# Optimization experiments

Hardware: AMD Instinct MI355X
Metric: run time of the kernel (lower is better)

Reference implementation:

```python
import jax, jax.numpy as jnp
import numpy as np

B, N, L = 256, 128, 2048
NF, AC, HID = 75, 3, 256
DIM, NHEAD, FPD, NWORD = 128, 8, 679, 8600


def setup_inputs() -> dict:
    key = jax.random.key(0)
    ks = iter(jax.random.split(key, 48))
    rn = lambda *s: jax.random.normal(next(ks), s, dtype=jnp.float32) * 0.05
    d = {}
    d['V'] = jax.random.normal(next(ks), (B, N, NF), dtype=jnp.float32)
    d['A'] = jax.random.uniform(next(ks), (B, AC, N, N), dtype=jnp.float32)
    d['fp'] = jax.random.uniform(next(ks), (B, FPD), dtype=jnp.float32)
    d['mol_size'] = jax.random.randint(next(ks), (B,), 1, N + 1, dtype=jnp.int32)
    d['protein_seq'] = jax.random.randint(next(ks), (B, L), 0, NWORD)
    d['label'] = jax.random.randint(next(ks), (B,), 0, 2)
    # GConv blocks (multi-channel GCN): 75->256, 256->256, 256->256
    d['gc_W1'], d['gc_b1'] = rn(AC, NF, HID), rn(HID)
    d['gc_W2'], d['gc_b2'] = rn(AC, HID, HID), rn(HID)
    d['gc_W3'], d['gc_b3'] = rn(AC, HID, HID), rn(HID)
    # fp linear chain: 679->128, 128->128
    d['fp_W1'], d['fp_b1'] = rn(FPD, DIM), rn(DIM)
    d['fp_W2'], d['fp_b2'] = rn(DIM, DIM), rn(DIM)
    # global attention pooling (per-head node scores) + readout
    d['att_W'] = rn(HID, NHEAD)
    d['ro_W'], d['ro_b'] = rn(HID * NHEAD, DIM), rn(DIM)
    d['emb'] = rn(NWORD, DIM)
    # cross-attention projections
    d['mfp_W'], d['mfp_b'] = rn(DIM, DIM), rn(DIM)
    d['pfp_W'], d['pfp_b'] = rn(DIM, DIM), rn(DIM)
    d['mv_W'], d['mv_b'] = rn(DIM, DIM), rn(DIM)
    d['pv_W'], d['pv_b'] = rn(DIM, DIM), rn(DIM)
    # stacked MLPs (3 layers each, width 2*dim)
    d['mlp1_W'], d['mlp1_b'] = rn(3, 2 * DIM, 2 * DIM), rn(3, 2 * DIM)
    d['mlp2_W'], d['mlp2_b'] = rn(3, 2 * DIM, 2 * DIM), rn(3, 2 * DIM)
    d['out1_W'], d['out1_b'] = rn(2 * DIM, 2), rn(2)
    d['out2_W'], d['out2_b'] = rn(2 * DIM, 2), rn(2)
    return d


def _gconv(V, A, W, b):
    # A: [b,c,n,m], V: [b,m,f], W: [c,f,o]
    AV = jnp.einsum('bcnm,bmf->bcnf', A, V)
    return jax.nn.relu(jnp.einsum('bcnf,cfo->bno', AV, W) + b)


def _cross_attn(hvec, prot_emb, mW, mb, pW, pb):
    # hvec: [b,d]; prot_emb: [b,l,d]
    h = jax.nn.relu(hvec @ mW + mb)                       # [b,d]
    hs = jax.nn.relu(jnp.einsum('bld,de->ble', prot_emb, pW) + pb)  # [b,l,d]
    w = jnp.tanh(jnp.einsum('bd,bld->bl', h, hs))         # [b,l]
    ys = w[..., None] * hs                                 # [b,l,d]
    return jnp.max(ys, axis=1)                             # [b,d]


def reference(V, A, fp, mol_size, protein_seq, label,
              gc_W1, gc_b1, gc_W2, gc_b2, gc_W3, gc_b3,
              fp_W1, fp_b1, fp_W2, fp_b2, att_W, ro_W, ro_b, emb,
              mfp_W, mfp_b, pfp_W, pfp_b, mv_W, mv_b, pv_W, pv_b,
              mlp1_W, mlp1_b, mlp2_W, mlp2_b, out1_W, out1_b, out2_W, out2_b):
    # fp linear chain (dropout = identity at inference)
    fp = jax.nn.relu(fp @ fp_W1 + fp_b1)
    fp = jax.nn.relu(fp @ fp_W2 + fp_b2)
    # graph conv blocks
    Vh = _gconv(V, A, gc_W1, gc_b1)
    Vh = _gconv(Vh, A, gc_W2, gc_b2)
    Vh = _gconv(Vh, A, gc_W3, gc_b3)
    # masked multi-head global attention pooling over nodes
    scores = jnp.einsum('bnf,fh->bnh', Vh, att_W)          # [b,n,heads]
    mask = jnp.arange(N)[None, :] < mol_size[:, None]       # [b,n]
    scores = jnp.where(mask[..., None], scores, -1e9)
    att = jax.nn.softmax(scores, axis=1)
    pooled = jnp.einsum('bnh,bnf->bhf', att, Vh).reshape(Vh.shape[0], -1)  # [b, heads*nf]
    Vr = jax.nn.relu(pooled @ ro_W + ro_b)                  # [b,dim]
    # protein embedding + ragged cross-attention branches
    prot_emb = emb[protein_seq]                             # [b,l,dim]
    itact1 = _cross_attn(fp, prot_emb, mfp_W, mfp_b, pfp_W, pfp_b)
    itact2 = _cross_attn(Vr, prot_emb, mv_W, mv_b, pv_W, pv_b)
    cat1 = jnp.concatenate([fp, itact1], axis=1)
    cat2 = jnp.concatenate([Vr, itact2], axis=1)
    for i in range(mlp1_W.shape[0]):
        cat1 = jax.nn.relu(cat1 @ mlp1_W[i] + mlp1_b[i])
        cat2 = jax.nn.relu(cat2 @ mlp2_W[i] + mlp2_b[i])
    pred_itact = (cat1 @ out1_W + out1_b) + (cat2 @ out2_W + out2_b)
    pred_labels = jnp.argmax(pred_itact, axis=1)
    pred_scores = jax.nn.softmax(pred_itact, axis=1)[:, 1]
    return (pred_itact, label, pred_labels, pred_scores)
```

## Files before the change

kernel.cpp:

```cpp
#include <hip/hip_runtime.h>
#include <math.h>

static constexpr int BB   = 256;
static constexpr int NN   = 128;
static constexpr int LL   = 2048;
static constexpr int NF   = 75;
static constexpr int AC   = 3;
static constexpr int HID  = 256;
static constexpr int DIM  = 128;
static constexpr int NHEAD= 8;
static constexpr int FPD  = 679;
static constexpr int FPDP = 704;
static constexpr int NWORD= 8600;
static constexpr int NWP  = 8704;
static constexpr int KB   = 768;

typedef __attribute__((ext_vector_type(8))) _Float16 f16x8;
typedef __attribute__((ext_vector_type(4))) float f32x4;
typedef unsigned int u32;
typedef unsigned short u16;

__device__ __forceinline__ u16 f2h(float x) {
    _Float16 h = (_Float16)x;
    return *(u16*)&h;
}
__device__ __forceinline__ u16 f2h_sat(float x) {
    x = fminf(fmaxf(x, -65000.f), 65000.f);
    _Float16 h = (_Float16)x;
    return *(u16*)&h;
}
__device__ __forceinline__ float h2f(u16 x) {
    return (float)(*(_Float16*)&x);
}

static constexpr float SC   = 0.0625f;
static constexpr float USC  = 16.0f;

__global__ __launch_bounds__(256)
void prepA_kernel(const float* __restrict__ A, u16* __restrict__ Ah)
{
    size_t base = (size_t)blockIdx.x * (NN * NN);
    int t = threadIdx.x;
    #pragma unroll
    for (int i = 0; i < 16; ++i) {
        int id = t + i * 256;
        float4 v = *(const float4*)(A + base + (size_t)id * 4);
        u32 p0 = (u32)f2h(v.x) | ((u32)f2h(v.y) << 16);
        u32 p1 = (u32)f2h(v.z) | ((u32)f2h(v.w) << 16);
        *(uint2*)(Ah + base + (size_t)id * 4) = make_uint2(p0, p1);
    }
}

__global__ __launch_bounds__(256)
void prepFp_kernel(const float* __restrict__ fp, u16* __restrict__ fph)
{
    int b = blockIdx.x, t = threadIdx.x;
    for (int i = t; i < FPDP; i += 256) {
        float v = (i < FPD) ? fp[(size_t)b * FPD + i] : 0.f;
        fph[(size_t)b * FPDP + i] = f2h(v);
    }
}

__global__ __launch_bounds__(256)
void prepFpW_kernel(const float* __restrict__ fpW1, const float* __restrict__ fpW2,
                    u16* __restrict__ W1t, u16* __restrict__ W2t)
{
    int o = blockIdx.x, z = blockIdx.y, t = threadIdx.x;
    if (z == 0) {
        for (int k = t; k < FPDP; k += 256) {
            float v = (k < FPD) ? fpW1[(size_t)k * DIM + o] : 0.f;
            W1t[(size_t)o * FPDP + k] = f2h(v);
        }
    } else {
        if (t < 128) W2t[(size_t)o * 128 + t] = f2h(fpW2[(size_t)t * DIM + o]);
    }
}

__global__ __launch_bounds__(128)
void prepCrossW_kernel(const float* __restrict__ pfpW, const float* __restrict__ pvW,
                       const float* __restrict__ mfpW, const float* __restrict__ mvW,
                       u16* __restrict__ pWt12, u16* __restrict__ mWt12)
{
    int o = blockIdx.x, z = blockIdx.y, t = threadIdx.x;
    const float* W = (z == 0) ? pfpW : (z == 1) ? pvW : (z == 2) ? mfpW : mvW;
    u16* Wt = (z < 2) ? (pWt12 + (size_t)z * 128 * 128)
                      : (mWt12 + (size_t)(z - 2) * 128 * 128);
    Wt[(size_t)o * 128 + t] = f2h(W[(size_t)t * 128 + o]);
}

__global__ __launch_bounds__(256)
void prepMlpW_kernel(const float* __restrict__ m1W, const float* __restrict__ m2W,
                     u16* __restrict__ Wmlp)
{
    int o = blockIdx.x, Lr = blockIdx.y, br = blockIdx.z, t = threadIdx.x;
    const float* W = (br ? m2W : m1W) + (size_t)Lr * 256 * 256;
    Wmlp[(((size_t)(br * 3 + Lr)) * 256 + o) * 256 + t] = f2h(W[(size_t)t * 256 + o]);
}

__global__ __launch_bounds__(256)
void fp1_mfma(const u16* __restrict__ fph, const u16* __restrict__ W1t,
              const float* __restrict__ b1, u16* __restrict__ FP1h)
{
    __shared__ u16 As[128 * 40];
    __shared__ u16 Bs[128 * 40];
    int mt = blockIdx.x;
    const u16* Ap = fph + (size_t)(mt * 128) * FPDP;

    int t = threadIdx.x;
    int l = t & 63, wid = t >> 6;
    int rb = (wid >> 1) * 64, cb = (wid & 1) * 64;
    int ln = l & 15, q = l >> 4;

    f32x4 acc[4][4] = {};

    for (int kt = 0; kt < FPDP / 32; ++kt) {
        #pragma unroll
        for (int i = 0; i < 2; ++i) {
            int id = t + i * 256;
            int row = id >> 2, qh = id & 3;
            *(uint4*)&As[row * 40 + qh * 8] =
                *(const uint4*)(Ap + (size_t)row * FPDP + kt * 32 + qh * 8);
            *(uint4*)&Bs[row * 40 + qh * 8] =
                *(const uint4*)(W1t + (size_t)row * FPDP + kt * 32 + qh * 8);
        }
        __syncthreads();
        f16x8 af[4], bfr[4];
        #pragma unroll
        for (int fr = 0; fr < 4; ++fr)
            af[fr] = *(const f16x8*)&As[(rb + fr * 16 + ln) * 40 + q * 8];
        #pragma unroll
        for (int fc = 0; fc < 4; ++fc)
            bfr[fc] = *(const f16x8*)&Bs[(cb + fc * 16 + ln) * 40 + q * 8];
        #pragma unroll
        for (int fr = 0; fr < 4; ++fr)
            #pragma unroll
            for (int fc = 0; fc < 4; ++fc)
                acc[fr][fc] = __builtin_amdgcn_mfma_f32_16x16x32_f16(
                    af[fr], bfr[fc], acc[fr][fc], 0, 0, 0);
        __syncthreads();
    }
    #pragma unroll
    for (int fr = 0; fr < 4; ++fr)
        #pragma unroll
        for (int fc = 0; fc < 4; ++fc) {
            int d = cb + fc * 16 + ln;
            float bv = b1[d];
            #pragma unroll
            for (int r = 0; r < 4; ++r) {
                int m = rb + fr * 16 + q * 4 + r;
                FP1h[(size_t)(mt * 128 + m) * 128 + d] = f2h(fmaxf(acc[fr][fc][r] + bv, 0.f));
            }
        }
}

__global__ __launch_bounds__(256)
void fp2_mfma(const u16* __restrict__ FP1h, const u16* __restrict__ W2t,
              const float* __restrict__ b2, float* __restrict__ FP2,
              u16* __restrict__ FP2h)
{
    __shared__ u16 As[128 * 40];
    __shared__ u16 Bs[128 * 40];
    int mt = blockIdx.x;
    const u16* Ap = FP1h + (size_t)(mt * 128) * 128;

    int t = threadIdx.x;
    int l = t & 63, wid = t >> 6;
    int rb = (wid >> 1) * 64, cb = (wid & 1) * 64;
    int ln = l & 15, q = l >> 4;

    f32x4 acc[4][4] = {};

    for (int kt = 0; kt < 4; ++kt) {
        #pragma unroll
        for (int i = 0; i < 2; ++i) {
            int id = t + i * 256;
            int row = id >> 2, qh = id & 3;
            *(uint4*)&As[row * 40 + qh * 8] =
                *(const uint4*)(Ap + (size_t)row * 128 + kt * 32 + qh * 8);
            *(uint4*)&Bs[row * 40 + qh * 8] =
                *(const uint4*)(W2t + (size_t)row * 128 + kt * 32 + qh * 8);
        }
        __syncthreads();
        f16x8 af[4], bfr[4];
        #pragma unroll
        for (int fr = 0; fr < 4; ++fr)
            af[fr] = *(const f16x8*)&As[(rb + fr * 16 + ln) * 40 + q * 8];
        #pragma unroll
        for (int fc = 0; fc < 4; ++fc)
            bfr[fc] = *(const f16x8*)&Bs[(cb + fc * 16 + ln) * 40 + q * 8];
        #pragma unroll
        for (int fr = 0; fr < 4; ++fr)
            #pragma unroll
            for (int fc = 0; fc < 4; ++fc)
                acc[fr][fc] = __builtin_amdgcn_mfma_f32_16x16x32_f16(
                    af[fr], bfr[fc], acc[fr][fc], 0, 0, 0);
        __syncthreads();
    }
    #pragma unroll
    for (int fr = 0; fr < 4; ++fr)
        #pragma unroll
        for (int fc = 0; fc < 4; ++fc) {
            int d = cb + fc * 16 + ln;
            float bv = b2[d];
            #pragma unroll
            for (int r = 0; r < 4; ++r) {
                int m = rb + fr * 16 + q * 4 + r;
                float val = fmaxf(acc[fr][fc][r] + bv, 0.f);
                FP2 [(size_t)(mt * 128 + m) * 128 + d] = val;
                FP2h[(size_t)(mt * 128 + m) * 128 + d] = f2h(val);
            }
        }
}

__global__ __launch_bounds__(256)
void hs12_mfma(const float* __restrict__ emb, const u16* __restrict__ pWt12,
               const float* __restrict__ ba, const float* __restrict__ bb_,
               u16* __restrict__ HS12)
{
    __shared__ u16 As[128 * 40];
    __shared__ u16 Bs[128 * 40];
    int ft = blockIdx.x, br = blockIdx.y;
    const u16* Bp = pWt12 + (size_t)br * 128 * 128;
    const float* bias = br ? bb_ : ba;
    int r0 = ft * 128;

    int t = threadIdx.x;
    int l = t & 63, wid = t >> 6;
    int rb = (wid >> 1) * 64, cb = (wid & 1) * 64;
    int ln = l & 15, q = l >> 4;

    f32x4 acc[4][4] = {};

    for (int kt = 0; kt < 4; ++kt) {
        #pragma unroll
        for (int i = 0; i < 4; ++i) {
            int id = t + i * 256;
            int row = id >> 3, qf = id & 7;
            int r = r0 + row;
            float4 v = make_float4(0.f, 0.f, 0.f, 0.f);
            if (r < NWORD) v = *(const float4*)(emb + (size_t)r * 128 + kt * 32 + qf * 4);
            u32 p0 = (u32)f2h(v.x) | ((u32)f2h(v.y) << 16);
            u32 p1 = (u32)f2h(v.z) | ((u32)f2h(v.w) << 16);
            u32* dst = (u32*)&As[row * 40 + qf * 4];
            dst[0] = p0; dst[1] = p1;
        }
        #pragma unroll
        for (int i = 0; i < 2; ++i) {
            int id = t + i * 256;
            int row = id >> 2, qh = id & 3;
            *(uint4*)&Bs[row * 40 + qh * 8] =
                *(const uint4*)(Bp + (size_t)row * 128 + kt * 32 + qh * 8);
        }
        __syncthreads();
        f16x8 af[4], bfr[4];
        #pragma unroll
        for (int fr = 0; fr < 4; ++fr)
            af[fr] = *(const f16x8*)&As[(rb + fr * 16 + ln) * 40 + q * 8];
        #pragma unroll
        for (int fc = 0; fc < 4; ++fc)
            bfr[fc] = *(const f16x8*)&Bs[(cb + fc * 16 + ln) * 40 + q * 8];
        #pragma unroll
        for (int fr = 0; fr < 4; ++fr)
            #pragma unroll
            for (int fc = 0; fc < 4; ++fc)
                acc[fr][fc] = __builtin_amdgcn_mfma_f32_16x16x32_f16(
                    af[fr], bfr[fc], acc[fr][fc], 0, 0, 0);
        __syncthreads();
    }
    #pragma unroll
    for (int fr = 0; fr < 4; ++fr)
        #pragma unroll
        for (int fc = 0; fc < 4; ++fc) {
            int d = cb + fc * 16 + ln;
            float bv = bias[d];
            #pragma unroll
            for (int r = 0; r < 4; ++r) {
                int m = rb + fr * 16 + q * 4 + r;
                int rr = r0 + m;
                if (rr < NWORD)
                    HS12[(size_t)rr * 256 + br * 128 + d] = f2h(fmaxf(acc[fr][fc][r] + bv, 0.f));
            }
        }
}

__global__ __launch_bounds__(256)
void prepVt_kernel(const float* __restrict__ V, u16* __restrict__ Vt)
{
    int b = blockIdx.x, t = threadIdx.x;
    __shared__ float sV[NN * NF];
    for (int i = t; i < NN * NF; i += 256) sV[i] = V[(size_t)b * (NN * NF) + i];
    __syncthreads();
    for (int i = t; i < 80 * 128; i += 256) {
        int f = i >> 7, n = i & 127;
        float v = (f < NF) ? sV[n * NF + f] : 0.f;
        Vt[(size_t)b * (80 * 128) + i] = f2h(v);
    }
}

__global__ __launch_bounds__(256)
void prepW_kernel(const float* __restrict__ W1, const float* __restrict__ W2,
                  const float* __restrict__ W3, u16* __restrict__ Wt1,
                  u16* __restrict__ Wt2, u16* __restrict__ Wt3)
{
    int o = blockIdx.x, z = blockIdx.y, t = threadIdx.x;
    if (z == 0) {
        int k = t;
        int c = k / 80, f = k - c * 80;
        float v = (c < 3 && f < NF) ? W1[((size_t)c * NF + f) * HID + o] : 0.f;
        Wt1[(size_t)o * 256 + k] = f2h(v);
    } else {
        const float* W = (z == 1) ? W2 : W3;
        u16* Wt = (z == 1) ? Wt2 : Wt3;
        for (int k = t; k < KB; k += 256) {
            int c = k >> 8, f = k & 255;
            Wt[(size_t)o * KB + k] = f2h(W[((size_t)c * HID + f) * HID + o]);
        }
    }
}

__global__ __launch_bounds__(256)
void transp_kernel(const u16* __restrict__ H, u16* __restrict__ Ht)
{
    __shared__ u16 s[32][34];
    int o0 = blockIdx.x * 32, n0 = blockIdx.y * 32, b = blockIdx.z;
    int tx = threadIdx.x & 31, ty = threadIdx.x >> 5;
    const u16* Hp = H + (size_t)b * (NN * HID);
    #pragma unroll
    for (int j = 0; j < 4; ++j)
        s[ty + 8 * j][tx] = Hp[(size_t)(n0 + ty + 8 * j) * HID + o0 + tx];
    __syncthreads();
    u16* Hto = Ht + (size_t)b * (HID * NN);
    #pragma unroll
    for (int j = 0; j < 4; ++j)
        Hto[(size_t)(o0 + ty + 8 * j) * NN + n0 + tx] = s[tx][ty + 8 * j];
}

__global__ __launch_bounds__(256)
void gA_mfma(const u16* __restrict__ Agr, const u16* __restrict__ Htr,
             u16* __restrict__ AV, int b0, int htStride, int fpMul, int Fvalid)
{
    __shared__ u16 As[128 * 40];
    __shared__ u16 Bs[128 * 40];
    int ft = blockIdx.x, c = blockIdx.y, bl = blockIdx.z;
    int b = b0 + bl;
    const u16* Ap = Agr + ((size_t)b * AC + c) * (NN * NN);
    const u16* Bp = Htr + (size_t)b * htStride + ft * (128 * 128);
    u16* Cp = AV + (size_t)bl * (NN * KB) + c * fpMul + ft * 128;

    int t = threadIdx.x;
    int l = t & 63, wid = t >> 6;
    int rb = (wid >> 1) * 64, cb = (wid & 1) * 64;
    int ln = l & 15, q = l >> 4;

    f32x4 acc[4][4] = {};

    for (int kt = 0; kt < 4; ++kt) {
        #pragma unroll
        for (int i = 0; i < 2; ++i) {
            int id = t + i * 256;
            int row = id >> 2, qh = id & 3;
            *(uint4*)&As[row * 40 + qh * 8] =
                *(const uint4*)(Ap + (size_t)row * NN + kt * 32 + qh * 8);
        }
        #pragma unroll
        for (int i = 0; i < 2; ++i) {
            int id = t + i * 256;
            int row = id >> 2, qh = id & 3;
            uint4 v = make_uint4(0, 0, 0, 0);
            if (row < Fvalid) v = *(const uint4*)(Bp + (size_t)row * 128 + kt * 32 + qh * 8);
            *(uint4*)&Bs[row * 40 + qh * 8] = v;
        }
        __syncthreads();
        f16x8 af[4], bfr[4];
        #pragma unroll
        for (int fr = 0; fr < 4; ++fr)
            af[fr] = *(const f16x8*)&As[(rb + fr * 16 + ln) * 40 + q * 8];
        #pragma unroll
        for (int fc = 0; fc < 4; ++fc)
            bfr[fc] = *(const f16x8*)&Bs[(cb + fc * 16 + ln) * 40 + q * 8];
        #pragma unroll
        for (int fr = 0; fr < 4; ++fr)
            #pragma unroll
            for (int fc = 0; fc < 4; ++fc)
                acc[fr][fc] = __builtin_amdgcn_mfma_f32_16x16x32_f16(
                    af[fr], bfr[fc], acc[fr][fc], 0, 0, 0);
        __syncthreads();
    }
    #pragma unroll
    for (int fr = 0; fr < 4; ++fr) {
        #pragma unroll
        for (int fc = 0; fc < 4; ++fc) {
            int fcol = cb + fc * 16 + ln;
            if (fcol < Fvalid) {
                #pragma unroll
                for (int r = 0; r < 4; ++r) {
                    int n = rb + fr * 16 + q * 4 + r;
                    Cp[(size_t)n * KB + fcol] = f2h_sat(acc[fr][fc][r] * SC);
                }
            }
        }
    }
}

__global__ __launch_bounds__(256)
void gB_mfma(const u16* __restrict__ AV, const u16* __restrict__ Wt,
             const float* __restrict__ bias, u16* __restrict__ H16,
             float* __restrict__ H32,
             int b0, int kTiles, int Ks, int outF32)
{
    __shared__ u16 As[128 * 40];
    __shared__ u16 Bs[128 * 40];
    int ot = blockIdx.x, bl = blockIdx.y;
    int b = b0 + bl;
    const u16* Ap = AV + (size_t)bl * (NN * KB);
    const u16* Bp = Wt + (size_t)ot * 128 * Ks;

    int t = threadIdx.x;
    int l = t & 63, wid = t >> 6;
    int rb = (wid >> 1) * 64, cb = (wid & 1) * 64;
    int ln = l & 15, q = l >> 4;

    f32x4 acc[4][4] = {};

    for (int kt = 0; kt < kTiles; ++kt) {
        #pragma unroll
        for (int i = 0; i < 2; ++i) {
            int id = t + i * 256;
            int row = id >> 2, qh = id & 3;
            *(uint4*)&As[row * 40 + qh * 8] =
                *(const uint4*)(Ap + (size_t)row * KB + kt * 32 + qh * 8);
            *(uint4*)&Bs[row * 40 + qh * 8] =
                *(const uint4*)(Bp + (size_t)row * Ks + kt * 32 + qh * 8);
        }
        __syncthreads();
        f16x8 af[4], bfr[4];
        #pragma unroll
        for (int fr = 0; fr < 4; ++fr)
            af[fr] = *(const f16x8*)&As[(rb + fr * 16 + ln) * 40 + q * 8];
        #pragma unroll
        for (int fc = 0; fc < 4; ++fc)
            bfr[fc] = *(const f16x8*)&Bs[(cb + fc * 16 + ln) * 40 + q * 8];
        #pragma unroll
        for (int fr = 0; fr < 4; ++fr)
            #pragma unroll
            for (int fc = 0; fc < 4; ++fc)
                acc[fr][fc] = __builtin_amdgcn_mfma_f32_16x16x32_f16(
                    af[fr], bfr[fc], acc[fr][fc], 0, 0, 0);
        __syncthreads();
    }
    #pragma unroll
    for (int fr = 0; fr < 4; ++fr) {
        #pragma unroll
        for (int fc = 0; fc < 4; ++fc) {
            int oc = cb + fc * 16 + ln;
            float bv = bias[ot * 128 + oc];
            #pragma unroll
            for (int r = 0; r < 4; ++r) {
                int n = rb + fr * 16 + q * 4 + r;
                float val = fmaxf(acc[fr][fc][r] * USC + bv, 0.f);
                if (outF32)
                    H32[((size_t)b * NN + n) * HID + ot * 128 + oc] = val;
                else
                    H16[((size_t)b * NN + n) * HID + ot * 128 + oc] = f2h_sat(val);
            }
        }
    }
}

__global__ __launch_bounds__(256)
void pool_kernel(const float* __restrict__ H3,
                 const float* __restrict__ attW,
                 const int* __restrict__ msz,
                 float* __restrict__ pooled)
{
    int b = blockIdx.x, t = threadIdx.x;
    __shared__ float sW[HID * NHEAD];
    __shared__ float sS[NN * NHEAD];
    __shared__ float sT[16][264];
    __shared__ float sP[16][NHEAD][2];
    for (int i = t; i < HID * NHEAD; i += 256) sW[i] = attW[i];
    __syncthreads();
    const float* Hb = H3 + (size_t)b * NN * HID;

    for (int n0 = 0; n0 < NN; n0 += 16) {
        for (int i = t; i < 16 * 64; i += 256) {
            int row = i >> 6, fq = (i & 63) * 4;
            float4 v = *(const float4*)(Hb + (size_t)(n0 + row) * HID + fq);
            *(float4*)&sT[row][fq] = v;
        }
        __syncthreads();
        {
            int nl = t >> 4, h = (t >> 1) & 7, fh = t & 1;
            float s = 0.f;
            for (int f = fh * 128; f < fh * 128 + 128; ++f)
                s += sT[nl][f] * sW[f * NHEAD + h];
            sP[nl][h][fh] = s;
        }
        __syncthreads();
        if (t < 128) {
            int n2 = t >> 3, h2 = t & 7;
            sS[(n0 + n2) * NHEAD + h2] = sP[n2][h2][0] + sP[n2][h2][1];
        }
        __syncthreads();
    }
    int ms = msz[b];
    int h = t >> 5, ln = t & 31;
    float mx = -1e9f;
    for (int n = ln; n < NN; n += 32) {
        float s = (n < ms) ? sS[n * NHEAD + h] : -1e9f;
        mx = fmaxf(mx, s);
    }
    #pragma unroll
    for (int off = 16; off; off >>= 1) mx = fmaxf(mx, __shfl_xor(mx, off, 32));
    float sum = 0.f;
    for (int n = ln; n < NN; n += 32) {
        float s = (n < ms) ? sS[n * NHEAD + h] : -1e9f;
        sum += expf(s - mx);
    }
    #pragma unroll
    for (int off = 16; off; off >>= 1) sum += __shfl_xor(sum, off, 32);
    float inv = 1.f / sum;
    for (int n = ln; n < NN; n += 32) {
        float s = (n < ms) ? sS[n * NHEAD + h] : -1e9f;
        sS[n * NHEAD + h] = expf(s - mx) * inv;
    }
    __syncthreads();
    float accp[NHEAD] = {};
    for (int n = 0; n < NN; ++n) {
        float hv = Hb[(size_t)n * HID + t];
        #pragma unroll
        for (int hh = 0; hh < NHEAD; ++hh) accp[hh] += sS[n * NHEAD + hh] * hv;
    }
    #pragma unroll
    for (int hh = 0; hh < NHEAD; ++hh)
        pooled[(size_t)b * (HID * NHEAD) + hh * HID + t] = accp[hh];
}

__global__ __launch_bounds__(128)
void readout_part(const float* __restrict__ pooled,
                  const float* __restrict__ roW,
                  float* __restrict__ Rp)
{
    int b = blockIdx.x, s = blockIdx.y, t = threadIdx.x;
    __shared__ float sx[256];
    const float* sp = pooled + (size_t)b * (HID * NHEAD) + s * 256;
    sx[t] = sp[t];
    sx[t + 128] = sp[t + 128];
    __syncthreads();
    float acc = 0.f;
    const float* W = roW + (size_t)(s * 256) * DIM + t;
    for (int k = 0; k < 256; ++k) acc += sx[k] * W[(size_t)k * DIM];
    Rp[((size_t)s * BB + b) * DIM + t] = acc;
}

__global__ __launch_bounds__(128)
void readout_merge(const float* __restrict__ Rp,
                   const float* __restrict__ rob,
                   float* __restrict__ Vr, u16* __restrict__ Vrh)
{
    int b = blockIdx.x, t = threadIdx.x;
    float a = rob[t];
    #pragma unroll
    for (int s = 0; s < 8; ++s) a += Rp[((size_t)s * BB + b) * DIM + t];
    float v = fmaxf(a, 0.f);
    Vr [(size_t)b * DIM + t] = v;
    Vrh[(size_t)b * DIM + t] = f2h_sat(v * SC);
}

__global__ __launch_bounds__(256)
void atth_mfma(const u16* __restrict__ FP2h, const u16* __restrict__ VRh,
               const u16* __restrict__ mWt12,
               const float* __restrict__ mfpb, const float* __restrict__ mvb,
               float* __restrict__ h1v, float* __restrict__ h2v)
{
    __shared__ u16 As[128 * 40];
    __shared__ u16 Bs[128 * 40];
    int mt = blockIdx.x, br = blockIdx.y;
    const u16* Ap = (br ? VRh : FP2h) + (size_t)(mt * 128) * 128;
    const u16* Bp = mWt12 + (size_t)br * 128 * 128;
    const float* bias = br ? mvb : mfpb;
    float unsc = br ? USC : 1.f;
    float* out = br ? h2v : h1v;

    int t = threadIdx.x;
    int l = t & 63, wid = t >> 6;
    int rb = (wid >> 1) * 64, cb = (wid & 1) * 64;
    int ln = l & 15, q = l >> 4;

    f32x4 acc[4][4] = {};

    for (int kt = 0; kt < 4; ++kt) {
        #pragma unroll
        for (int i = 0; i < 2; ++i) {
            int id = t + i * 256;
            int row = id >> 2, qh = id & 3;
            *(uint4*)&As[row * 40 + qh * 8] =
                *(const uint4*)(Ap + (size_t)row * 128 + kt * 32 + qh * 8);
            *(uint4*)&Bs[row * 40 + qh * 8] =
                *(const uint4*)(Bp + (size_t)row * 128 + kt * 32 + qh * 8);
        }
        __syncthreads();
        f16x8 af[4], bfr[4];
        #pragma unroll
        for (int fr = 0; fr < 4; ++fr)
            af[fr] = *(const f16x8*)&As[(rb + fr * 16 + ln) * 40 + q * 8];
        #pragma unroll
        for (int fc = 0; fc < 4; ++fc)
            bfr[fc] = *(const f16x8*)&Bs[(cb + fc * 16 + ln) * 40 + q * 8];
        #pragma unroll
        for (int fr = 0; fr < 4; ++fr)
            #pragma unroll
            for (int fc = 0; fc < 4; ++fc)
                acc[fr][fc] = __builtin_amdgcn_mfma_f32_16x16x32_f16(
                    af[fr], bfr[fc], acc[fr][fc], 0, 0, 0);
        __syncthreads();
    }
    #pragma unroll
    for (int fr = 0; fr < 4; ++fr)
        #pragma unroll
        for (int fc = 0; fc < 4; ++fc) {
            int d = cb + fc * 16 + ln;
            float bv = bias[d];
            #pragma unroll
            for (int r = 0; r < 4; ++r) {
                int m = rb + fr * 16 + q * 4 + r;
                out[(size_t)(mt * 128 + m) * 128 + d] = fmaxf(acc[fr][fc][r] * unsc + bv, 0.f);
            }
        }
}

__global__ __launch_bounds__(256)
void cross_part_kernel(const int* __restrict__ seq,
                       const u16* __restrict__ HS12,
                       const float* __restrict__ h1v, const float* __restrict__ h2v,
                       float* __restrict__ Pc)
{
    int b = blockIdx.x, s = blockIdx.y, t = threadIdx.x;
    int g = t >> 4, gl = t & 15;
    int d0 = gl * 8;
    float h1[8], h2[8];
    #pragma unroll
    for (int j = 0; j < 8; ++j) {
        h1[j] = h1v[(size_t)b * DIM + d0 + j];
        h2[j] = h2v[(size_t)b * DIM + d0 + j];
    }
    float m1[8], m2[8];
    #pragma unroll
    for (int j = 0; j < 8; ++j) { m1[j] = -INFINITY; m2[j] = -INFINITY; }
    const int* sq = seq + (size_t)b * LL + s * 256;
    for (int it = 0; it < 16; ++it) {
        int tok = sq[g + 16 * it];
        const u16* r12 = HS12 + (size_t)tok * 256 + d0;
        f16x8 va16 = *(const f16x8*)(r12);
        f16x8 vb16 = *(const f16x8*)(r12 + 128);
        float va[8], vb[8];
        float p1 = 0.f, p2 = 0.f;
        #pragma unroll
        for (int j = 0; j < 8; ++j) {
            va[j] = (float)va16[j];
            vb[j] = (float)vb16[j];
            p1 += h1[j] * va[j];
            p2 += h2[j] * vb[j];
        }
        #pragma unroll
        for (int off = 8; off; off >>= 1) {
            p1 += __shfl_xor(p1, off);
            p2 += __shfl_xor(p2, off);
        }
        float w1 = tanhf(p1), w2 = tanhf(p2);
        #pragma unroll
        for (int j = 0; j < 8; ++j) {
            m1[j] = fmaxf(m1[j], w1 * va[j]);
            m2[j] = fmaxf(m2[j], w2 * vb[j]);
        }
    }
    __shared__ float red[16][2][DIM];
    #pragma unroll
    for (int j = 0; j < 8; ++j) { red[g][0][d0 + j] = m1[j]; red[g][1][d0 + j] = m2[j]; }
    __syncthreads();
    int tb = t >> 7, d = t & 127;
    float mx = red[0][tb][d];
    #pragma unroll
    for (int gg = 1; gg < 16; ++gg) mx = fmaxf(mx, red[gg][tb][d]);
    Pc[(((size_t)s * BB + b) * 2 + tb) * DIM + d] = mx;
}

__global__ __launch_bounds__(256)
void cross_merge_kernel(const float* __restrict__ Pc,
                        float* __restrict__ IT1, float* __restrict__ IT2)
{
    int b = blockIdx.x, t = threadIdx.x;
    float m = -INFINITY;
    for (int s = 0; s < 8; ++s)
        m = fmaxf(m, Pc[((size_t)s * BB + b) * 256 + t]);
    if (t < DIM) IT1[(size_t)b * DIM + t] = m;
    else         IT2[(size_t)b * DIM + t - DIM] = m;
}

__global__ __launch_bounds__(256)
void prepX_kernel(const float* __restrict__ FP2, const float* __restrict__ VR,
                  const float* __restrict__ IT1, const float* __restrict__ IT2,
                  u16* __restrict__ Xh)
{
    int b = blockIdx.x, br = blockIdx.y, t = threadIdx.x;
    const float* a0 = br ? VR : FP2;
    const float* a1 = br ? IT2 : IT1;
    float v = (t < 128) ? a0[(size_t)b * 128 + t] : a1[(size_t)b * 128 + t - 128];
    Xh[((size_t)br * BB + b) * 256 + t] = f2h_sat(v * SC);
}

__global__ __launch_bounds__(256)
void mlpL_mfma(const u16* __restrict__ X, const u16* __restrict__ Wmlp,
               const float* __restrict__ m1b, const float* __restrict__ m2b,
               int Lr, u16* __restrict__ Y)
{
    __shared__ u16 As[128 * 40];
    __shared__ u16 Bs[128 * 40];
    int mt = blockIdx.x, ot = blockIdx.y, br = blockIdx.z;
    const u16* Ap = X + ((size_t)br * BB + mt * 128) * 256;
    const u16* Bp = Wmlp + (((size_t)(br * 3 + Lr)) * 256 + ot * 128) * 256;
    const float* bias = (br ? m2b : m1b) + (size_t)Lr * 256 + ot * 128;

    int t = threadIdx.x;
    int l = t & 63, wid = t >> 6;
    int rb = (wid >> 1) * 64, cb = (wid & 1) * 64;
    int ln = l & 15, q = l >> 4;

    f32x4 acc[4][4] = {};

    for (int kt = 0; kt < 8; ++kt) {
        #pragma unroll
        for (int i = 0; i < 2; ++i) {
            int id = t + i * 256;
            int row = id >> 2, qh = id & 3;
            *(uint4*)&As[row * 40 + qh * 8] =
                *(const uint4*)(Ap + (size_t)row * 256 + kt * 32 + qh * 8);
            *(uint4*)&Bs[row * 40 + qh * 8] =
                *(const uint4*)(Bp + (size_t)row * 256 + kt * 32 + qh * 8);
        }
        __syncthreads();
        f16x8 af[4], bfr[4];
        #pragma unroll
        for (int fr = 0; fr < 4; ++fr)
            af[fr] = *(const f16x8*)&As[(rb + fr * 16 + ln) * 40 + q * 8];
        #pragma unroll
        for (int fc = 0; fc < 4; ++fc)
            bfr[fc] = *(const f16x8*)&Bs[(cb + fc * 16 + ln) * 40 + q * 8];
        #pragma unroll
        for (int fr = 0; fr < 4; ++fr)
            #pragma unroll
            for (int fc = 0; fc < 4; ++fc)
                acc[fr][fc] = __builtin_amdgcn_mfma_f32_16x16x32_f16(
                    af[fr], bfr[fc], acc[fr][fc], 0, 0, 0);
        __syncthreads();
    }
    #pragma unroll
    for (int fr = 0; fr < 4; ++fr)
        #pragma unroll
        for (int fc = 0; fc < 4; ++fc) {
            int oc = cb + fc * 16 + ln;
            float bv = bias[oc] * SC;
            #pragma unroll
            for (int r = 0; r < 4; ++r) {
                int m = rb + fr * 16 + q * 4 + r;
                Y[((size_t)br * BB + (mt * 128 + m)) * 256 + ot * 128 + oc] =
                    f2h_sat(fmaxf(acc[fr][fc][r] + bv, 0.f));
            }
        }
}

__global__ __launch_bounds__(256)
void mlp_out_kernel(const u16* __restrict__ Y,
                    const float* __restrict__ o1W, const float* __restrict__ o1b,
                    const float* __restrict__ o2W, const float* __restrict__ o2b,
                    const int* __restrict__ label,
                    float* __restrict__ dout)
{
    int b = blockIdx.x, t = threadIdx.x;
    __shared__ float pl[2][128];
    const u16* y1 = Y + (size_t)b * 256;
    const u16* y2 = Y + ((size_t)BB + b) * 256;
    int j = t & 1, k2 = t >> 1;
    float p = USC * (h2f(y1[k2])       * o1W[k2 * 2 + j]
                   + h2f(y1[k2 + 128]) * o1W[(k2 + 128) * 2 + j]
                   + h2f(y2[k2])       * o2W[k2 * 2 + j]
                   + h2f(y2[k2 + 128]) * o2W[(k2 + 128) * 2 + j]);
    pl[j][k2] = p;
    __syncthreads();
    for (int s = 64; s > 0; s >>= 1) {
        if (k2 < s) pl[j][k2] += pl[j][k2 + s];
        __syncthreads();
    }
    if (t == 0) {
        float l0 = pl[0][0] + o1b[0] + o2b[0];
        float l1 = pl[1][0] + o1b[1] + o2b[1];
        dout[(size_t)b * 2 + 0] = l0;
        dout[(size_t)b * 2 + 1] = l1;
        dout[2 * BB + b] = (float)label[b];
        dout[3 * BB + b] = (float)((l1 > l0) ? 1 : 0);
        float mx = fmaxf(l0, l1);
        float e0 = expf(l0 - mx), e1 = expf(l1 - mx);
        dout[4 * BB + b] = e1 / (e0 + e1);
    }
}

extern "C" void kernel_launch(void* const* d_in, const int* in_sizes, int n_in,
                              void* d_out, int out_size, void* d_ws, size_t ws_size,
                              hipStream_t stream)
{
    const float* V    = (const float*)d_in[0];
    const float* A    = (const float*)d_in[1];
    const float* fp   = (const float*)d_in[2];
    const int*   msz  = (const int*)  d_in[3];
    const int*   seq  = (const int*)  d_in[4];
    const int*   lab  = (const int*)  d_in[5];
    const float* gcW1 = (const float*)d_in[6];  const float* gcb1 = (const float*)d_in[7];
    const float* gcW2 = (const float*)d_in[8];  const float* gcb2 = (const float*)d_in[9];
    const float* gcW3 = (const float*)d_in[10]; const float* gcb3 = (const float*)d_in[11];
    const float* fpW1 = (const float*)d_in[12]; const float* fpb1 = (const float*)d_in[13];
    const float* fpW2 = (const float*)d_in[14]; const float* fpb2 = (const float*)d_in[15];
    const float* attW = (const float*)d_in[16];
    const float* roW  = (const float*)d_in[17]; const float* rob  = (const float*)d_in[18];
    const float* emb  = (const float*)d_in[19];
    const float* mfpW = (const float*)d_in[20]; const float* mfpb = (const float*)d_in[21];
    const float* pfpW = (const float*)d_in[22]; const float* pfpb = (const float*)d_in[23];
    const float* mvW  = (const float*)d_in[24]; const float* mvb  = (const float*)d_in[25];
    const float* pvW  = (const float*)d_in[26]; const float* pvb  = (const float*)d_in[27];
    const float* m1W  = (const float*)d_in[28]; const float* m1b  = (const float*)d_in[29];
    const float* m2W  = (const float*)d_in[30]; const float* m2b  = (const float*)d_in[31];
    const float* o1W  = (const float*)d_in[32]; const float* o1b  = (const float*)d_in[33];
    const float* o2W  = (const float*)d_in[34]; const float* o2b  = (const float*)d_in[35];
    float* dout = (float*)d_out;

    char* ws = (char*)d_ws;
    size_t off = 0;
    auto alloc = [&](size_t bytes) -> char* {
        char* p = ws + off;
        off += (bytes + 255) & ~(size_t)255;
        return p;
    };
    u16*   Ah    = (u16*)  alloc((size_t)BB * AC * NN * NN * 2);
    u16*   Vt    = (u16*)  alloc((size_t)BB * 80 * 128 * 2);
    u16*   Wt1   = (u16*)  alloc((size_t)256 * 256 * 2);
    u16*   Wt2   = (u16*)  alloc((size_t)256 * KB * 2);
    u16*   Wt3   = (u16*)  alloc((size_t)256 * KB * 2);
    u16*   H16   = (u16*)  alloc((size_t)BB * NN * HID * 2);
    float* H3f   = (float*)alloc((size_t)BB * NN * HID * 4);
    u16*   Ht    = (u16*)  alloc((size_t)BB * HID * NN * 2);
    u16*   fph   = (u16*)  alloc((size_t)BB * FPDP * 2);
    u16*   W1t   = (u16*)  alloc((size_t)DIM * FPDP * 2);
    u16*   W2t   = (u16*)  alloc((size_t)DIM * DIM * 2);
    u16*   FP1h  = (u16*)  alloc((size_t)BB * DIM * 2);
    float* FP2   = (float*)alloc((size_t)BB * DIM * 4);
    u16*   FP2h  = (u16*)  alloc((size_t)BB * DIM * 2);
    u16*   pWt12 = (u16*)  alloc((size_t)2 * 128 * 128 * 2);
    u16*   mWt12 = (u16*)  alloc((size_t)2 * 128 * 128 * 2);
    u16*   HS12  = (u16*)  alloc((size_t)NWP * 256 * 2);
    float* PO    = (float*)alloc((size_t)BB * HID * NHEAD * 4);
    float* VR    = (float*)alloc((size_t)BB * DIM * 4);
    u16*   VRh   = (u16*)  alloc((size_t)BB * DIM * 2);
    float* H1V   = (float*)alloc((size_t)BB * DIM * 4);
    float* H2V   = (float*)alloc((size_t)BB * DIM * 4);
    float* IT1   = (float*)alloc((size_t)BB * DIM * 4);
    float* IT2   = (float*)alloc((size_t)BB * DIM * 4);
    float* Pc    = (float*)alloc((size_t)8 * BB * 2 * DIM * 4);
    float* Rp    = (float*)alloc((size_t)8 * BB * DIM * 4);
    u16*   Wmlp  = (u16*)  alloc((size_t)2 * 3 * 256 * 256 * 2);
    u16*   Xa    = (u16*)  alloc((size_t)2 * BB * 256 * 2);
    u16*   Xb    = (u16*)  alloc((size_t)2 * BB * 256 * 2);
    size_t fixedBytes = off;

    int CB = 8;
    size_t perB = (size_t)NN * KB * 2;
    {
        const int tiers[] = {256, 128, 64, 32, 16, 8, 4, 2, 1};
        for (int i = 0; i < 9; ++i)
            if (fixedBytes + (size_t)tiers[i] * perB <= ws_size) { CB = tiers[i]; break; }
    }
    u16* AV = (u16*)(ws + fixedBytes);

    prepA_kernel<<<BB * AC, 256, 0, stream>>>(A, Ah);
    prepVt_kernel<<<BB, 256, 0, stream>>>(V, Vt);
    prepW_kernel<<<dim3(256, 3), 256, 0, stream>>>(gcW1, gcW2, gcW3, Wt1, Wt2, Wt3);
    prepFp_kernel<<<BB, 256, 0, stream>>>(fp, fph);
    prepFpW_kernel<<<dim3(128, 2), 256, 0, stream>>>(fpW1, fpW2, W1t, W2t);
    prepCrossW_kernel<<<dim3(128, 4), 128, 0, stream>>>(pfpW, pvW, mfpW, mvW, pWt12, mWt12);
    prepMlpW_kernel<<<dim3(256, 3, 2), 256, 0, stream>>>(m1W, m2W, Wmlp);
    fp1_mfma<<<2, 256, 0, stream>>>(fph, W1t, fpb1, FP1h);
    fp2_mfma<<<2, 256, 0, stream>>>(FP1h, W2t, fpb2, FP2, FP2h);
    hs12_mfma<<<dim3(NWP / 128, 2), 256, 0, stream>>>(emb, pWt12, pfpb, pvb, HS12);

    for (int b0 = 0; b0 < BB; b0 += CB) {
        gA_mfma<<<dim3(1, AC, CB), 256, 0, stream>>>(Ah, Vt, AV, b0, 80 * 128, 80, 80);
        gB_mfma<<<dim3(2, CB), 256, 0, stream>>>(AV, Wt1, gcb1, H16, H3f, b0, 8, 256, 0);
    }
    transp_kernel<<<dim3(8, 4, BB), 256, 0, stream>>>(H16, Ht);
    for (int b0 = 0; b0 < BB; b0 += CB) {
        gA_mfma<<<dim3(2, AC, CB), 256, 0, stream>>>(Ah, Ht, AV, b0, HID * NN, 256, 128);
        gB_mfma<<<dim3(2, CB), 256, 0, stream>>>(AV, Wt2, gcb2, H16, H3f, b0, 24, KB, 0);
    }
    transp_kernel<<<dim3(8, 4, BB), 256, 0, stream>>>(H16, Ht);
    for (int b0 = 0; b0 < BB; b0 += CB) {
        gA_mfma<<<dim3(2, AC, CB), 256, 0, stream>>>(Ah, Ht, AV, b0, HID * NN, 256, 128);
        gB_mfma<<<dim3(2, CB), 256, 0, stream>>>(AV, Wt3, gcb3, H16, H3f, b0, 24, KB, 1);
    }

    pool_kernel<<<BB, 256, 0, stream>>>(H3f, attW, msz, PO);
    readout_part<<<dim3(BB, 8), 128, 0, stream>>>(PO, roW, Rp);
    readout_merge<<<BB, 128, 0, stream>>>(Rp, rob, VR, VRh);
    atth_mfma<<<dim3(2, 2), 256, 0, stream>>>(FP2h, VRh, mWt12, mfpb, mvb, H1V, H2V);
    cross_part_kernel<<<dim3(BB, 8), 256, 0, stream>>>(seq, HS12, H1V, H2V, Pc);
    cross_merge_kernel<<<BB, 256, 0, stream>>>(Pc, IT1, IT2);
    prepX_kernel<<<dim3(BB, 2), 256, 0, stream>>>(FP2, VR, IT1, IT2, Xa);
    mlpL_mfma<<<dim3(2, 2, 2), 256, 0, stream>>>(Xa, Wmlp, m1b, m2b, 0, Xb);
    mlpL_mfma<<<dim3(2, 2, 2), 256, 0, stream>>>(Xb, Wmlp, m1b, m2b, 1, Xa);
    mlpL_mfma<<<dim3(2, 2, 2), 256, 0, stream>>>(Xa, Wmlp, m1b, m2b, 2, Xb);
    mlp_out_kernel<<<BB, 256, 0, stream>>>(Xb, o1W, o1b, o2W, o2b, lab, dout);
}
```

Baseline: 535.9 us.

## Fuse transpose into GCN epilogue and store final layer output in fp16

The gB GEMM epilogue now writes its output already transposed through an LDS tile, so the two standalone transpose kernels are removed. The last GCN layer writes scaled fp16 instead of fp32, halving that write and the pool kernel's read. The pool kernel stages the whole per-batch fp16 tile in LDS once and rescales afterwards. This trades extra LDS use (a 34 KB epilogue tile and a 66 KB pool tile) and fp16 precision on the final activations for less global memory traffic and fewer launches.

```diff
diff --git a/kernel.cpp b/kernel.cpp
--- a/kernel.cpp
+++ b/kernel.cpp
@@ -319,23 +319,6 @@
 }
 
 __global__ __launch_bounds__(256)
-void transp_kernel(const u16* __restrict__ H, u16* __restrict__ Ht)
-{
-    __shared__ u16 s[32][34];
-    int o0 = blockIdx.x * 32, n0 = blockIdx.y * 32, b = blockIdx.z;
-    int tx = threadIdx.x & 31, ty = threadIdx.x >> 5;
-    const u16* Hp = H + (size_t)b * (NN * HID);
-    #pragma unroll
-    for (int j = 0; j < 4; ++j)
-        s[ty + 8 * j][tx] = Hp[(size_t)(n0 + ty + 8 * j) * HID + o0 + tx];
-    __syncthreads();
-    u16* Hto = Ht + (size_t)b * (HID * NN);
-    #pragma unroll
-    for (int j = 0; j < 4; ++j)
-        Hto[(size_t)(o0 + ty + 8 * j) * NN + n0 + tx] = s[tx][ty + 8 * j];
-}
-
-__global__ __launch_bounds__(256)
 void gA_mfma(const u16* __restrict__ Agr, const u16* __restrict__ Htr,
              u16* __restrict__ AV, int b0, int htStride, int fpMul, int Fvalid)
 {
@@ -404,12 +387,12 @@
 
 __global__ __launch_bounds__(256)
 void gB_mfma(const u16* __restrict__ AV, const u16* __restrict__ Wt,
-             const float* __restrict__ bias, u16* __restrict__ H16,
-             float* __restrict__ H32,
-             int b0, int kTiles, int Ks, int outF32)
+             const float* __restrict__ bias, u16* __restrict__ Hout,
+             int b0, int kTiles, int Ks, int mode)
 {
     __shared__ u16 As[128 * 40];
     __shared__ u16 Bs[128 * 40];
+    __shared__ u16 sLT[128][136];
     int ot = blockIdx.x, bl = blockIdx.y;
     int b = b0 + bl;
     const u16* Ap = AV + (size_t)bl * (NN * KB);
@@ -448,58 +431,70 @@
                     af[fr], bfr[fc], acc[fr][fc], 0, 0, 0);
         __syncthreads();
     }
-    #pragma unroll
-    for (int fr = 0; fr < 4; ++fr) {
-        #pragma unroll
-        for (int fc = 0; fc < 4; ++fc) {
-            int oc = cb + fc * 16 + ln;
-            float bv = bias[ot * 128 + oc];
-            #pragma unroll
-            for (int r = 0; r < 4; ++r) {
-                int n = rb + fr * 16 + q * 4 + r;
-                float val = fmaxf(acc[fr][fc][r] * USC + bv, 0.f);
-                if (outF32)
-                    H32[((size_t)b * NN + n) * HID + ot * 128 + oc] = val;
-                else
-                    H16[((size_t)b * NN + n) * HID + ot * 128 + oc] = f2h_sat(val);
+    if (mode == 0) {
+        #pragma unroll
+        for (int fr = 0; fr < 4; ++fr)
+            #pragma unroll
+            for (int fc = 0; fc < 4; ++fc) {
+                int oc = cb + fc * 16 + ln;
+                float bv = bias[ot * 128 + oc];
+                #pragma unroll
+                for (int r = 0; r < 4; ++r) {
+                    int n = rb + fr * 16 + q * 4 + r;
+                    sLT[oc][n] = f2h_sat(fmaxf(acc[fr][fc][r] * USC + bv, 0.f));
+                }
             }
-        }
-    }
-}
-
-__global__ __launch_bounds__(256)
-void pool_kernel(const float* __restrict__ H3,
+        __syncthreads();
+        int row = t >> 1, half = t & 1;
+        u16* dst = Hout + ((size_t)b * HID + ot * 128 + row) * NN + half * 64;
+        #pragma unroll
+        for (int j = 0; j < 8; ++j)
+            *(uint4*)(dst + j * 8) = *(const uint4*)&sLT[row][half * 64 + j * 8];
+    } else {
+        #pragma unroll
+        for (int fr = 0; fr < 4; ++fr)
+            #pragma unroll
+            for (int fc = 0; fc < 4; ++fc) {
+                int oc = cb + fc * 16 + ln;
+                float bv = bias[ot * 128 + oc];
+                #pragma unroll
+                for (int r = 0; r < 4; ++r) {
+                    int n = rb + fr * 16 + q * 4 + r;
+                    float val = fmaxf(acc[fr][fc][r] * USC + bv, 0.f);
+                    Hout[((size_t)b * NN + n) * HID + ot * 128 + oc] = f2h_sat(val * SC);
+                }
+            }
+    }
+}
+
+__global__ __launch_bounds__(256)
+void pool_kernel(const u16* __restrict__ H3h,
                  const float* __restrict__ attW,
                  const int* __restrict__ msz,
                  float* __restrict__ pooled)
 {
     int b = blockIdx.x, t = threadIdx.x;
+    __shared__ u16  sTh[128][264];
     __shared__ float sW[HID * NHEAD];
     __shared__ float sS[NN * NHEAD];
-    __shared__ float sT[16][264];
     __shared__ float sP[16][NHEAD][2];
     for (int i = t; i < HID * NHEAD; i += 256) sW[i] = attW[i];
+    const u16* Hb = H3h + (size_t)b * NN * HID;
+    for (int i = t; i < 128 * 32; i += 256) {
+        int row = i >> 5, fq = (i & 31) * 8;
+        *(uint4*)&sTh[row][fq] = *(const uint4*)(Hb + (size_t)row * HID + fq);
+    }
     __syncthreads();
-    const float* Hb = H3 + (size_t)b * NN * HID;
-
     for (int n0 = 0; n0 < NN; n0 += 16) {
-        for (int i = t; i < 16 * 64; i += 256) {
-            int row = i >> 6, fq = (i & 63) * 4;
-            float4 v = *(const float4*)(Hb + (size_t)(n0 + row) * HID + fq);
-            *(float4*)&sT[row][fq] = v;
-        }
-        __syncthreads();
-        {
-            int nl = t >> 4, h = (t >> 1) & 7, fh = t & 1;
-            float s = 0.f;
-            for (int f = fh * 128; f < fh * 128 + 128; ++f)
-                s += sT[nl][f] * sW[f * NHEAD + h];
-            sP[nl][h][fh] = s;
-        }
+        int nl = t >> 4, h = (t >> 1) & 7, fh = t & 1;
+        float s = 0.f;
+        for (int f = fh * 128; f < fh * 128 + 128; ++f)
+            s += h2f(sTh[n0 + nl][f]) * sW[f * NHEAD + h];
+        sP[nl][h][fh] = s;
         __syncthreads();
         if (t < 128) {
             int n2 = t >> 3, h2 = t & 7;
-            sS[(n0 + n2) * NHEAD + h2] = sP[n2][h2][0] + sP[n2][h2][1];
+            sS[(n0 + n2) * NHEAD + h2] = USC * (sP[n2][h2][0] + sP[n2][h2][1]);
         }
         __syncthreads();
     }
@@ -527,13 +522,13 @@
     __syncthreads();
     float accp[NHEAD] = {};
     for (int n = 0; n < NN; ++n) {
-        float hv = Hb[(size_t)n * HID + t];
+        float hv = h2f(sTh[n][t]);
         #pragma unroll
         for (int hh = 0; hh < NHEAD; ++hh) accp[hh] += sS[n * NHEAD + hh] * hv;
     }
     #pragma unroll
     for (int hh = 0; hh < NHEAD; ++hh)
-        pooled[(size_t)b * (HID * NHEAD) + hh * HID + t] = accp[hh];
+        pooled[(size_t)b * (HID * NHEAD) + hh * HID + t] = USC * accp[hh];
 }
 
 __global__ __launch_bounds__(128)
@@ -844,9 +839,8 @@
     u16*   Wt1   = (u16*)  alloc((size_t)256 * 256 * 2);
     u16*   Wt2   = (u16*)  alloc((size_t)256 * KB * 2);
     u16*   Wt3   = (u16*)  alloc((size_t)256 * KB * 2);
-    u16*   H16   = (u16*)  alloc((size_t)BB * NN * HID * 2);
-    float* H3f   = (float*)alloc((size_t)BB * NN * HID * 4);
     u16*   Ht    = (u16*)  alloc((size_t)BB * HID * NN * 2);
+    u16*   H3h   = (u16*)  alloc((size_t)BB * NN * HID * 2);
     u16*   fph   = (u16*)  alloc((size_t)BB * FPDP * 2);
     u16*   W1t   = (u16*)  alloc((size_t)DIM * FPDP * 2);
     u16*   W2t   = (u16*)  alloc((size_t)DIM * DIM * 2);
@@ -892,20 +886,18 @@
 
     for (int b0 = 0; b0 < BB; b0 += CB) {
         gA_mfma<<<dim3(1, AC, CB), 256, 0, stream>>>(Ah, Vt, AV, b0, 80 * 128, 80, 80);
-        gB_mfma<<<dim3(2, CB), 256, 0, stream>>>(AV, Wt1, gcb1, H16, H3f, b0, 8, 256, 0);
-    }
-    transp_kernel<<<dim3(8, 4, BB), 256, 0, stream>>>(H16, Ht);
+        gB_mfma<<<dim3(2, CB), 256, 0, stream>>>(AV, Wt1, gcb1, Ht, b0, 8, 256, 0);
+    }
     for (int b0 = 0; b0 < BB; b0 += CB) {
         gA_mfma<<<dim3(2, AC, CB), 256, 0, stream>>>(Ah, Ht, AV, b0, HID * NN, 256, 128);
-        gB_mfma<<<dim3(2, CB), 256, 0, stream>>>(AV, Wt2, gcb2, H16, H3f, b0, 24, KB, 0);
-    }
-    transp_kernel<<<dim3(8, 4, BB), 256, 0, stream>>>(H16, Ht);
+        gB_mfma<<<dim3(2, CB), 256, 0, stream>>>(AV, Wt2, gcb2, Ht, b0, 24, KB, 0);
+    }
     for (int b0 = 0; b0 < BB; b0 += CB) {
         gA_mfma<<<dim3(2, AC, CB), 256, 0, stream>>>(Ah, Ht, AV, b0, HID * NN, 256, 128);
-        gB_mfma<<<dim3(2, CB), 256, 0, stream>>>(AV, Wt3, gcb3, H16, H3f, b0, 24, KB, 1);
-    }
-
-    pool_kernel<<<BB, 256, 0, stream>>>(H3f, attW, msz, PO);
+        gB_mfma<<<dim3(2, CB), 256, 0, stream>>>(AV, Wt3, gcb3, H3h, b0, 24, KB, 1);
+    }
+
+    pool_kernel<<<BB, 256, 0, stream>>>(H3h, attW, msz, PO);
     readout_part<<<dim3(BB, 8), 128, 0, stream>>>(PO, roW, Rp);
     readout_merge<<<BB, 128, 0, stream>>>(Rp, rob, VR, VRh);
     atth_mfma<<<dim3(2, 2), 256, 0, stream>>>(FP2h, VRh, mWt12, mfpb, mvb, H1V, H2V);
```

Result: faster. 507.6 us (-5.3%).
